# Optimization experiments

Measured on AMD Instinct MI355X. Metric: run time of the kernel, lower is better.

## Reference

```python
import jax, jax.numpy as jnp
import numpy as np

ITERATIONS = 3  # init_kwargs: adjacency power order

def setup_inputs() -> dict:
    key = jax.random.key(0)
    ks = jax.random.split(key, 8)
    n_nodes = 100000
    in_ch, out_ch = 512, 128
    nnz_feat = 1600000
    n_edges = 1600000
    feat_rows = jax.random.randint(ks[0], (nnz_feat,), 0, n_nodes, dtype=jnp.int32)
    feat_cols = jax.random.randint(ks[1], (nnz_feat,), 0, in_ch, dtype=jnp.int32)
    feat_values = jax.random.uniform(ks[2], (nnz_feat,), dtype=jnp.float32)
    adj_rows = jax.random.randint(ks[3], (n_edges,), 0, n_nodes, dtype=jnp.int32)
    adj_cols = jax.random.randint(ks[4], (n_edges,), 0, n_nodes, dtype=jnp.int32)
    # normalized adjacency values (positive, roughly 1/degree scale)
    adj_values = jax.random.uniform(ks[5], (n_edges,), dtype=jnp.float32) / 16.0
    # xavier-uniform-like init
    bound_w = float(np.sqrt(6.0 / (in_ch + out_ch)))
    weight = jax.random.uniform(ks[6], (in_ch, out_ch), minval=-bound_w, maxval=bound_w, dtype=jnp.float32)
    bound_b = float(np.sqrt(6.0 / (1 + out_ch)))
    bias = jax.random.uniform(ks[7], (1, out_ch), minval=-bound_b, maxval=bound_b, dtype=jnp.float32)
    return {"feat_rows": feat_rows, "feat_cols": feat_cols, "feat_values": feat_values,
            "adj_rows": adj_rows, "adj_cols": adj_cols, "adj_values": adj_values,
            "weight": weight, "bias": bias, "n_nodes": n_nodes}

def reference(feat_rows, feat_cols, feat_values, adj_rows, adj_cols, adj_values, weight, bias, n_nodes):
    # SpMM: (sparse features [n_nodes, in_ch]) @ weight [in_ch, out_ch]
    # base[r] = sum over nnz with row r of val * weight[col]
    contrib = feat_values[:, None] * weight[feat_cols]           # [nnz, out_ch]
    base = jax.ops.segment_sum(contrib, feat_rows, num_segments=n_nodes)  # [n_nodes, out_ch]
    # bias + dropout (eval mode: identity) + relu
    base = jax.nn.relu(base + bias)
    # iterative sparse propagation: base = A_norm @ base, (iterations - 1) times
    for _ in range(ITERATIONS - 1):
        msgs = adj_values[:, None] * base[adj_cols]              # [n_edges, out_ch]
        base = jax.ops.segment_sum(msgs, adj_rows, num_segments=n_nodes)
    return base
```

## Files before the change

kernel.cpp:

```cpp
#include <hip/hip_runtime.h>
#include <hip/hip_fp16.h>


#define CH 128
#define BR 128
#define SCAN_BLK 1024
#define BIN_WGS 256
#define BIN_THR 512


__global__ void bucket_hist_kernel(const int* __restrict__ rows, int* __restrict__ bcounts,
                                   int nE, int nbuck, int chunk) {
    extern __shared__ int hcnt[];
    const int tid = threadIdx.x;
    const long long T = blockDim.x;
    long long start = (long long)blockIdx.x * chunk;
    long long end = start + chunk;
    if (end > nE) end = nE;
    for (int b = tid; b < nbuck; b += blockDim.x) hcnt[b] = 0;
    __syncthreads();
    if (start < end) {
        long long i = start + tid;
        for (; i + 3 * T < end; i += 4 * T) {
            int r0 = rows[i], r1 = rows[i + T], r2 = rows[i + 2 * T], r3 = rows[i + 3 * T];
            atomicAdd(&hcnt[r0 >> 7], 1);
            atomicAdd(&hcnt[r1 >> 7], 1);
            atomicAdd(&hcnt[r2 >> 7], 1);
            atomicAdd(&hcnt[r3 >> 7], 1);
        }
        for (; i < end; i += T) atomicAdd(&hcnt[rows[i] >> 7], 1);
    }
    __syncthreads();
    for (int b = tid; b < nbuck; b += blockDim.x) {
        int c = hcnt[b];
        if (c) atomicAdd(&bcounts[b], c);
    }
}

__global__ void bucket_scan_kernel(const int* __restrict__ bcounts, int* __restrict__ bcur,
                                   int* __restrict__ bucket_base, int* __restrict__ row_ptr_n,
                                   int nbuck) {
    __shared__ int lds[SCAN_BLK];
    int tid = threadIdx.x;
    int x = (tid < nbuck) ? bcounts[tid] : 0;
    lds[tid] = x;
    __syncthreads();
    for (int off = 1; off < SCAN_BLK; off <<= 1) {
        int y = (tid >= off) ? lds[tid - off] : 0;
        __syncthreads();
        lds[tid] += y;
        __syncthreads();
    }
    if (tid < nbuck) {
        int excl = lds[tid] - x;
        bcur[tid] = excl;
        bucket_base[tid] = excl;
    }
    if (tid == nbuck - 1) {
        bucket_base[nbuck] = lds[tid];
        *row_ptr_n = lds[tid];
    }
}

__global__ void multisplit_bin_kernel(const int* __restrict__ rows, const int* __restrict__ cols,
                                      const float* __restrict__ vals, int* __restrict__ bcur,
                                      int2* __restrict__ cv_tmp, int nE, int nbuck, int chunk) {
    extern __shared__ int lds[];
    int* hcnt  = lds;
    int* hbase = lds + nbuck;
    const int tid = threadIdx.x;
    const long long T = blockDim.x;
    long long start = (long long)blockIdx.x * chunk;
    long long end = start + chunk;
    if (end > nE) end = nE;
    if (start >= end) return;

    for (int b = tid; b < nbuck; b += blockDim.x) hcnt[b] = 0;
    __syncthreads();
    {
        long long i = start + tid;
        for (; i + 3 * T < end; i += 4 * T) {
            int r0 = rows[i], r1 = rows[i + T], r2 = rows[i + 2 * T], r3 = rows[i + 3 * T];
            atomicAdd(&hcnt[r0 >> 7], 1);
            atomicAdd(&hcnt[r1 >> 7], 1);
            atomicAdd(&hcnt[r2 >> 7], 1);
            atomicAdd(&hcnt[r3 >> 7], 1);
        }
        for (; i < end; i += T) atomicAdd(&hcnt[rows[i] >> 7], 1);
    }
    __syncthreads();
    for (int b = tid; b < nbuck; b += blockDim.x) {
        int c = hcnt[b];
        hbase[b] = c ? atomicAdd(&bcur[b], c) : 0;
        hcnt[b] = 0;
    }
    __syncthreads();
    {
        long long i = start + tid;
        for (; i + 3 * T < end; i += 4 * T) {
            int r0 = rows[i], r1 = rows[i + T], r2 = rows[i + 2 * T], r3 = rows[i + 3 * T];
            int c0 = cols[i], c1 = cols[i + T], c2 = cols[i + 2 * T], c3 = cols[i + 3 * T];
            float v0 = vals[i], v1 = vals[i + T], v2 = vals[i + 2 * T], v3 = vals[i + 3 * T];
            int b0 = r0 >> 7, b1 = r1 >> 7, b2 = r2 >> 7, b3 = r3 >> 7;
            int p0 = hbase[b0] + atomicAdd(&hcnt[b0], 1);
            int p1 = hbase[b1] + atomicAdd(&hcnt[b1], 1);
            int p2 = hbase[b2] + atomicAdd(&hcnt[b2], 1);
            int p3 = hbase[b3] + atomicAdd(&hcnt[b3], 1);
            cv_tmp[p0] = make_int2(c0 | ((r0 & (BR - 1)) << 24), __float_as_int(v0));
            cv_tmp[p1] = make_int2(c1 | ((r1 & (BR - 1)) << 24), __float_as_int(v1));
            cv_tmp[p2] = make_int2(c2 | ((r2 & (BR - 1)) << 24), __float_as_int(v2));
            cv_tmp[p3] = make_int2(c3 | ((r3 & (BR - 1)) << 24), __float_as_int(v3));
        }
        for (; i < end; i += T) {
            int r = rows[i];
            int b = r >> 7;
            int p = hbase[b] + atomicAdd(&hcnt[b], 1);
            cv_tmp[p] = make_int2(cols[i] | ((r & (BR - 1)) << 24), __float_as_int(vals[i]));
        }
    }
}

__global__ void reorder2_kernel(const int* __restrict__ bucket_base,
                                const int2* __restrict__ cv_tmp, int2* __restrict__ cv,
                                int* __restrict__ row_ptr, int n) {
    __shared__ int cnt[BR];
    __shared__ int tmp[BR];
    int b = blockIdx.x;
    int rbase = b * BR;
    int tid = threadIdx.x;
    int s = bucket_base[b], e = bucket_base[b + 1];
    if (tid < BR) cnt[tid] = 0;
    __syncthreads();
    for (int i = s + tid; i < e; i += blockDim.x)
        atomicAdd(&cnt[((unsigned)cv_tmp[i].x) >> 24], 1);
    __syncthreads();
    if (tid < BR) tmp[tid] = cnt[tid];
    __syncthreads();
    for (int off = 1; off < BR; off <<= 1) {
        int y = 0;
        if (tid < BR && tid >= off) y = tmp[tid - off];
        __syncthreads();
        if (tid < BR) tmp[tid] += y;
        __syncthreads();
    }
    if (tid < BR) {
        int excl = s + tmp[tid] - cnt[tid];
        if (rbase + tid < n) row_ptr[rbase + tid] = excl;
        cnt[tid] = excl;
    }
    __syncthreads();
    for (int i = s + tid; i < e; i += blockDim.x) {
        int2 ent = cv_tmp[i];
        int rl = ((unsigned)ent.x) >> 24;
        int p = atomicAdd(&cnt[rl], 1);
        cv[p] = make_int2(ent.x & 0x00FFFFFF, ent.y);
    }
}


__global__ void wconv_kernel(const float* __restrict__ W, __half2* __restrict__ Wh, int n2) {
    int i = blockIdx.x * blockDim.x + threadIdx.x;
    if (i < n2) Wh[i] = __float22half2_rn(reinterpret_cast<const float2*>(W)[i]);
}


__global__ void spmm_g4_kernel(const int* __restrict__ row_ptr,
                               const long long* __restrict__ cv,
                               const __half2* __restrict__ Wh,
                               const float* __restrict__ bias,
                               __half2* __restrict__ outh, int n) {
    __shared__ long long sc[4 * 64];
    int gtid = blockIdx.x * blockDim.x + threadIdx.x;
    int wid = gtid >> 6;
    int lane = gtid & 63;
    if (wid >= n) return;
    int g = lane >> 4;
    int cl = lane & 15;
    long long* mysc = sc + (threadIdx.x >> 6) * 64;
    int s = row_ptr[wid], e = row_ptr[wid + 1];
    float acc0 = 0.f, acc1 = 0.f, acc2 = 0.f, acc3 = 0.f;
    float acc4 = 0.f, acc5 = 0.f, acc6 = 0.f, acc7 = 0.f;
    for (int base = s; base < e; base += 64) {
        int idx = base + lane;
        mysc[lane] = (idx < e) ? cv[idx] : 0;
        int m = e - base; if (m > 64) m = 64;
        for (int k0 = 0; k0 < m; k0 += 4) {
            long long ck = mysc[k0 + g];
            int col = (int)ck;
            float v = __int_as_float((int)(ck >> 32));
            float4 wv = *reinterpret_cast<const float4*>(Wh + (long long)col * 64 + cl * 4);
            float2 f0 = __half22float2(*reinterpret_cast<const __half2*>(&wv.x));
            float2 f1 = __half22float2(*reinterpret_cast<const __half2*>(&wv.y));
            float2 f2 = __half22float2(*reinterpret_cast<const __half2*>(&wv.z));
            float2 f3 = __half22float2(*reinterpret_cast<const __half2*>(&wv.w));
            acc0 += v * f0.x; acc1 += v * f0.y;
            acc2 += v * f1.x; acc3 += v * f1.y;
            acc4 += v * f2.x; acc5 += v * f2.y;
            acc6 += v * f3.x; acc7 += v * f3.y;
        }
    }
    acc0 += __shfl_xor(acc0, 16); acc1 += __shfl_xor(acc1, 16);
    acc2 += __shfl_xor(acc2, 16); acc3 += __shfl_xor(acc3, 16);
    acc4 += __shfl_xor(acc4, 16); acc5 += __shfl_xor(acc5, 16);
    acc6 += __shfl_xor(acc6, 16); acc7 += __shfl_xor(acc7, 16);
    acc0 += __shfl_xor(acc0, 32); acc1 += __shfl_xor(acc1, 32);
    acc2 += __shfl_xor(acc2, 32); acc3 += __shfl_xor(acc3, 32);
    acc4 += __shfl_xor(acc4, 32); acc5 += __shfl_xor(acc5, 32);
    acc6 += __shfl_xor(acc6, 32); acc7 += __shfl_xor(acc7, 32);
    if (g == 0) {
        const float4* bp = reinterpret_cast<const float4*>(bias);
        float4 b0 = bp[cl * 2], b1 = bp[cl * 2 + 1];
        acc0 = fmaxf(acc0 + b0.x, 0.f); acc1 = fmaxf(acc1 + b0.y, 0.f);
        acc2 = fmaxf(acc2 + b0.z, 0.f); acc3 = fmaxf(acc3 + b0.w, 0.f);
        acc4 = fmaxf(acc4 + b1.x, 0.f); acc5 = fmaxf(acc5 + b1.y, 0.f);
        acc6 = fmaxf(acc6 + b1.z, 0.f); acc7 = fmaxf(acc7 + b1.w, 0.f);
        __half2 h0 = __floats2half2_rn(acc0, acc1);
        __half2 h1 = __floats2half2_rn(acc2, acc3);
        __half2 h2 = __floats2half2_rn(acc4, acc5);
        __half2 h3 = __floats2half2_rn(acc6, acc7);
        float4 ov;
        *reinterpret_cast<__half2*>(&ov.x) = h0;
        *reinterpret_cast<__half2*>(&ov.y) = h1;
        *reinterpret_cast<__half2*>(&ov.z) = h2;
        *reinterpret_cast<__half2*>(&ov.w) = h3;
        *reinterpret_cast<float4*>(outh + (long long)wid * 64 + cl * 4) = ov;
    }
}

__global__ void prop_csr_h2h_kernel(const int* __restrict__ row_ptr,
                                    const long long* __restrict__ cv,
                                    const __half2* __restrict__ src, __half2* __restrict__ dst,
                                    int n) {
    __shared__ long long sc[4 * 64];
    int gtid = blockIdx.x * blockDim.x + threadIdx.x;
    int wid = gtid >> 6;
    int lane = gtid & 63;
    if (wid >= n) return;
    long long* mysc = sc + (threadIdx.x >> 6) * 64;
    int s = row_ptr[wid], e = row_ptr[wid + 1];
    float2 acc = {0.0f, 0.0f};
    for (int base = s; base < e; base += 64) {
        int idx = base + lane;
        mysc[lane] = (idx < e) ? cv[idx] : 0;
        int m = e - base; if (m > 64) m = 64;
        for (int k0 = 0; k0 < m; k0 += 8) {
            #pragma unroll
            for (int j = 0; j < 8; j++) {
                long long ck = mysc[k0 + j];
                int col = (int)ck;
                float v = __int_as_float((int)(ck >> 32));
                float2 xf = __half22float2(src[(long long)col * 64 + lane]);
                acc.x += v * xf.x; acc.y += v * xf.y;
            }
        }
    }
    dst[(long long)wid * 64 + lane] = __float22half2_rn(acc);
}

__global__ void prop_csr_h2f_kernel(const int* __restrict__ row_ptr,
                                    const long long* __restrict__ cv,
                                    const __half2* __restrict__ src, float* __restrict__ dst,
                                    int n) {
    __shared__ long long sc[4 * 64];
    int gtid = blockIdx.x * blockDim.x + threadIdx.x;
    int wid = gtid >> 6;
    int lane = gtid & 63;
    if (wid >= n) return;
    long long* mysc = sc + (threadIdx.x >> 6) * 64;
    int s = row_ptr[wid], e = row_ptr[wid + 1];
    float2 acc = {0.0f, 0.0f};
    for (int base = s; base < e; base += 64) {
        int idx = base + lane;
        mysc[lane] = (idx < e) ? cv[idx] : 0;
        int m = e - base; if (m > 64) m = 64;
        for (int k0 = 0; k0 < m; k0 += 8) {
            #pragma unroll
            for (int j = 0; j < 8; j++) {
                long long ck = mysc[k0 + j];
                int col = (int)ck;
                float v = __int_as_float((int)(ck >> 32));
                float2 xf = __half22float2(src[(long long)col * 64 + lane]);
                acc.x += v * xf.x; acc.y += v * xf.y;
            }
        }
    }
    reinterpret_cast<float2*>(dst)[(long long)wid * 64 + lane] = acc;
}


__global__ void bias_relu_kernel(float* __restrict__ buf, const float* __restrict__ bias,
                                 long long total) {
    long long i = ((long long)blockIdx.x * blockDim.x + threadIdx.x) * 4;
    if (i >= total) return;
    float4 v = *reinterpret_cast<float4*>(buf + i);
    int ch = (int)(i & (CH - 1));
    float4 b = *reinterpret_cast<const float4*>(bias + ch);
    v.x = fmaxf(v.x + b.x, 0.0f);
    v.y = fmaxf(v.y + b.y, 0.0f);
    v.z = fmaxf(v.z + b.z, 0.0f);
    v.w = fmaxf(v.w + b.w, 0.0f);
    *reinterpret_cast<float4*>(buf + i) = v;
}

__global__ void spmm_scatter_kernel(const int* __restrict__ rows, const int* __restrict__ cols,
                                    const float* __restrict__ vals, const float* __restrict__ weight,
                                    float* __restrict__ out, int nnz) {
    long long tid = (long long)blockIdx.x * blockDim.x + threadIdx.x;
    if (tid >= (long long)nnz * 32) return;
    int e = (int)(tid >> 5), lane = (int)(tid & 31);
    int r = rows[e], c = cols[e];
    float v = vals[e];
    const float4 w = *reinterpret_cast<const float4*>(weight + (long long)c * CH + lane * 4);
    float* dst = out + (long long)r * CH + lane * 4;
    unsafeAtomicAdd(dst + 0, v * w.x);
    unsafeAtomicAdd(dst + 1, v * w.y);
    unsafeAtomicAdd(dst + 2, v * w.z);
    unsafeAtomicAdd(dst + 3, v * w.w);
}

__global__ void prop_scatter_kernel(const int* __restrict__ rows, const int* __restrict__ cols,
                                    const float* __restrict__ vals, const float* __restrict__ src,
                                    float* __restrict__ dst, int ne) {
    long long tid = (long long)blockIdx.x * blockDim.x + threadIdx.x;
    if (tid >= (long long)ne * 32) return;
    int e = (int)(tid >> 5), lane = (int)(tid & 31);
    int r = rows[e], c = cols[e];
    float v = vals[e];
    const float4 s = *reinterpret_cast<const float4*>(src + (long long)c * CH + lane * 4);
    float* d = dst + (long long)r * CH + lane * 4;
    unsafeAtomicAdd(d + 0, v * s.x);
    unsafeAtomicAdd(d + 1, v * s.y);
    unsafeAtomicAdd(d + 2, v * s.z);
    unsafeAtomicAdd(d + 3, v * s.w);
}


static inline size_t align64(size_t x) { return (x + 63) & ~(size_t)63; }

extern "C" void kernel_launch(void* const* d_in, const int* in_sizes, int n_in,
                              void* d_out, int out_size, void* d_ws, size_t ws_size,
                              hipStream_t stream) {
    const int*   feat_rows = (const int*)d_in[0];
    const int*   feat_cols = (const int*)d_in[1];
    const float* feat_vals = (const float*)d_in[2];
    const int*   adj_rows  = (const int*)d_in[3];
    const int*   adj_cols  = (const int*)d_in[4];
    const float* adj_vals  = (const float*)d_in[5];
    const float* weight    = (const float*)d_in[6];
    const float* bias      = (const float*)d_in[7];

    const int nnz = in_sizes[0];
    const int ne  = in_sizes[3];
    const int n   = out_size / CH;
    const int in_ch = in_sizes[6] / CH;

    float* out = (float*)d_out;
    char*  ws  = (char*)d_ws;

    const size_t NBF = (size_t)n * CH * sizeof(float);
    const size_t NBH = (size_t)n * CH * sizeof(__half);
    const long long total_elems = (long long)n * CH;
    const int BLK = 256;
    const int ew_blocks = (int)((total_elems / 4 + BLK - 1) / BLK);
    const int maxe = nnz > ne ? nnz : ne;
    const int nbuck = (n + BR - 1) / BR;
    const size_t bin_lds = (size_t)nbuck * 2 * sizeof(int);

    size_t off = 0;
    __half2* baseh   = (__half2*)(ws + off); off += align64(NBH);
    __half2* pingh   = (__half2*)(ws + off); off += align64(NBH);
    int*   row_ptr  = (int*)(ws + off);   off += align64(((size_t)n + 1) * 4);
    int*   bcounts  = (int*)(ws + off);   off += align64((size_t)nbuck * 4);
    int*   bcur     = (int*)(ws + off);   off += align64((size_t)nbuck * 4);
    int*   bbase    = (int*)(ws + off);   off += align64(((size_t)nbuck + 1) * 4);
    __half2* Wh     = (__half2*)(ws + off); off += align64((size_t)in_ch * 64 * 4);
    int2*  cv       = (int2*)(ws + off);  off += align64((size_t)maxe * 8);
    int2*  cv_tmp   = (int2*)pingh;
    const bool fast = (ws_size >= off) && (nbuck <= SCAN_BLK) &&
                      (n <= (1 << 24)) && (bin_lds <= 64 * 1024) &&
                      (in_ch <= (1 << 22)) &&
                      ((size_t)maxe * 8 <= NBH);

    if (fast) {
        const int row_blocks = (int)(((long long)n * 64 + BLK - 1) / BLK);
        const int chunk_feat = (nnz + BIN_WGS - 1) / BIN_WGS;
        const int chunk_adj  = (ne + BIN_WGS - 1) / BIN_WGS;
        const int w2 = in_ch * 64;
        const size_t hist_lds = (size_t)nbuck * sizeof(int);

        wconv_kernel<<<(w2 + BLK - 1) / BLK, BLK, 0, stream>>>(weight, Wh, w2);

        hipMemsetAsync(bcounts, 0, (size_t)nbuck * 4, stream);
        bucket_hist_kernel<<<BIN_WGS, BIN_THR, hist_lds, stream>>>(
            feat_rows, bcounts, nnz, nbuck, chunk_feat);
        bucket_scan_kernel<<<1, SCAN_BLK, 0, stream>>>(bcounts, bcur, bbase, row_ptr + n, nbuck);
        multisplit_bin_kernel<<<BIN_WGS, BIN_THR, bin_lds, stream>>>(
            feat_rows, feat_cols, feat_vals, bcur, cv_tmp, nnz, nbuck, chunk_feat);
        reorder2_kernel<<<nbuck, BIN_THR, 0, stream>>>(bbase, cv_tmp, cv, row_ptr, n);
        spmm_g4_kernel<<<row_blocks, BLK, 0, stream>>>(
            row_ptr, (const long long*)cv, Wh, bias, baseh, n);

        hipMemsetAsync(bcounts, 0, (size_t)nbuck * 4, stream);
        bucket_hist_kernel<<<BIN_WGS, BIN_THR, hist_lds, stream>>>(
            adj_rows, bcounts, ne, nbuck, chunk_adj);
        bucket_scan_kernel<<<1, SCAN_BLK, 0, stream>>>(bcounts, bcur, bbase, row_ptr + n, nbuck);
        multisplit_bin_kernel<<<BIN_WGS, BIN_THR, bin_lds, stream>>>(
            adj_rows, adj_cols, adj_vals, bcur, cv_tmp, ne, nbuck, chunk_adj);
        reorder2_kernel<<<nbuck, BIN_THR, 0, stream>>>(bbase, cv_tmp, cv, row_ptr, n);
        prop_csr_h2h_kernel<<<row_blocks, BLK, 0, stream>>>(
            row_ptr, (const long long*)cv, baseh, pingh, n);
        prop_csr_h2f_kernel<<<row_blocks, BLK, 0, stream>>>(
            row_ptr, (const long long*)cv, pingh, out, n);
    } else {
        float* ping = (float*)ws;
        const int spmm_blocks = (int)(((long long)nnz * 32 + BLK - 1) / BLK);
        const int prop_blocks = (int)(((long long)ne * 32 + BLK - 1) / BLK);
        hipMemsetAsync(d_out, 0, NBF, stream);
        spmm_scatter_kernel<<<spmm_blocks, BLK, 0, stream>>>(feat_rows, feat_cols, feat_vals,
                                                             weight, out, nnz);
        bias_relu_kernel<<<ew_blocks, BLK, 0, stream>>>(out, bias, total_elems);
        hipMemsetAsync(ping, 0, NBF, stream);
        prop_scatter_kernel<<<prop_blocks, BLK, 0, stream>>>(adj_rows, adj_cols, adj_vals,
                                                             out, ping, ne);
        hipMemsetAsync(d_out, 0, NBF, stream);
        prop_scatter_kernel<<<prop_blocks, BLK, 0, stream>>>(adj_rows, adj_cols, adj_vals,
                                                             ping, out, ne);
    }
}
```

Before: 259.1 us.

## Store per-workgroup bucket histograms and use 4-edge-per-wave propagation kernels

The binning pipeline now writes per-workgroup bucket histograms and scans them per bucket with wave shuffles. The multisplit kernel can then take deterministic offsets directly instead of rebuilding its histogram and doing global atomics. This removes a full second pass over the row indices, two memsets and the atomic contention. The propagation kernels now split each wave into four groups of 16 lanes that each handle a different edge with 16-byte vector loads, followed by a cross-group shuffle reduction. This gives more independent gathers in flight, at the cost of an extra wgscan launch and the shuffle reduction.

Result: faster. 253.2 us (-2.3%).

```diff
diff --git a/kernel.cpp b/kernel.cpp
--- a/kernel.cpp
+++ b/kernel.cpp
@@ -9,7 +9,7 @@
 #define BIN_THR 512
 
 
-__global__ void bucket_hist_kernel(const int* __restrict__ rows, int* __restrict__ bcounts,
+__global__ void bucket_hist_kernel(const int* __restrict__ rows, int* __restrict__ wg_counts,
                                    int nE, int nbuck, int chunk) {
     extern __shared__ int hcnt[];
     const int tid = threadIdx.x;
@@ -31,13 +31,32 @@
         for (; i < end; i += T) atomicAdd(&hcnt[rows[i] >> 7], 1);
     }
     __syncthreads();
-    for (int b = tid; b < nbuck; b += blockDim.x) {
-        int c = hcnt[b];
-        if (c) atomicAdd(&bcounts[b], c);
-    }
-}
-
-__global__ void bucket_scan_kernel(const int* __restrict__ bcounts, int* __restrict__ bcur,
+    for (int b = tid; b < nbuck; b += blockDim.x)
+        wg_counts[(long long)blockIdx.x * nbuck + b] = hcnt[b];
+}
+
+__global__ void wgscan_kernel(int* __restrict__ wg_counts, int* __restrict__ bcounts,
+                              int nbuck, int nwg) {
+    int b = blockIdx.x * (blockDim.x >> 6) + (threadIdx.x >> 6);
+    int lane = threadIdx.x & 63;
+    if (b >= nbuck) return;
+    int carry = 0;
+    for (int base = 0; base < nwg; base += 64) {
+        int wg = base + lane;
+        int v = (wg < nwg) ? wg_counts[(long long)wg * nbuck + b] : 0;
+        int x = v;
+        #pragma unroll
+        for (int off = 1; off < 64; off <<= 1) {
+            int y = __shfl_up(x, off);
+            if (lane >= off) x += y;
+        }
+        if (wg < nwg) wg_counts[(long long)wg * nbuck + b] = carry + x - v;
+        carry += __shfl(x, 63);
+    }
+    if (lane == 0) bcounts[b] = carry;
+}
+
+__global__ void bucket_scan_kernel(const int* __restrict__ bcounts,
                                    int* __restrict__ bucket_base, int* __restrict__ row_ptr_n,
                                    int nbuck) {
     __shared__ int lds[SCAN_BLK];
@@ -51,11 +70,7 @@
         lds[tid] += y;
         __syncthreads();
     }
-    if (tid < nbuck) {
-        int excl = lds[tid] - x;
-        bcur[tid] = excl;
-        bucket_base[tid] = excl;
-    }
+    if (tid < nbuck) bucket_base[tid] = lds[tid] - x;
     if (tid == nbuck - 1) {
         bucket_base[nbuck] = lds[tid];
         *row_ptr_n = lds[tid];
@@ -63,7 +78,9 @@
 }
 
 __global__ void multisplit_bin_kernel(const int* __restrict__ rows, const int* __restrict__ cols,
-                                      const float* __restrict__ vals, int* __restrict__ bcur,
+                                      const float* __restrict__ vals,
+                                      const int* __restrict__ bbase,
+                                      const int* __restrict__ wg_counts,
                                       int2* __restrict__ cv_tmp, int nE, int nbuck, int chunk) {
     extern __shared__ int lds[];
     int* hcnt  = lds;
@@ -73,50 +90,32 @@
     long long start = (long long)blockIdx.x * chunk;
     long long end = start + chunk;
     if (end > nE) end = nE;
+    for (int b = tid; b < nbuck; b += blockDim.x) {
+        hbase[b] = bbase[b] + wg_counts[(long long)blockIdx.x * nbuck + b];
+        hcnt[b] = 0;
+    }
+    __syncthreads();
     if (start >= end) return;
-
-    for (int b = tid; b < nbuck; b += blockDim.x) hcnt[b] = 0;
-    __syncthreads();
-    {
-        long long i = start + tid;
-        for (; i + 3 * T < end; i += 4 * T) {
-            int r0 = rows[i], r1 = rows[i + T], r2 = rows[i + 2 * T], r3 = rows[i + 3 * T];
-            atomicAdd(&hcnt[r0 >> 7], 1);
-            atomicAdd(&hcnt[r1 >> 7], 1);
-            atomicAdd(&hcnt[r2 >> 7], 1);
-            atomicAdd(&hcnt[r3 >> 7], 1);
-        }
-        for (; i < end; i += T) atomicAdd(&hcnt[rows[i] >> 7], 1);
-    }
-    __syncthreads();
-    for (int b = tid; b < nbuck; b += blockDim.x) {
-        int c = hcnt[b];
-        hbase[b] = c ? atomicAdd(&bcur[b], c) : 0;
-        hcnt[b] = 0;
-    }
-    __syncthreads();
-    {
-        long long i = start + tid;
-        for (; i + 3 * T < end; i += 4 * T) {
-            int r0 = rows[i], r1 = rows[i + T], r2 = rows[i + 2 * T], r3 = rows[i + 3 * T];
-            int c0 = cols[i], c1 = cols[i + T], c2 = cols[i + 2 * T], c3 = cols[i + 3 * T];
-            float v0 = vals[i], v1 = vals[i + T], v2 = vals[i + 2 * T], v3 = vals[i + 3 * T];
-            int b0 = r0 >> 7, b1 = r1 >> 7, b2 = r2 >> 7, b3 = r3 >> 7;
-            int p0 = hbase[b0] + atomicAdd(&hcnt[b0], 1);
-            int p1 = hbase[b1] + atomicAdd(&hcnt[b1], 1);
-            int p2 = hbase[b2] + atomicAdd(&hcnt[b2], 1);
-            int p3 = hbase[b3] + atomicAdd(&hcnt[b3], 1);
-            cv_tmp[p0] = make_int2(c0 | ((r0 & (BR - 1)) << 24), __float_as_int(v0));
-            cv_tmp[p1] = make_int2(c1 | ((r1 & (BR - 1)) << 24), __float_as_int(v1));
-            cv_tmp[p2] = make_int2(c2 | ((r2 & (BR - 1)) << 24), __float_as_int(v2));
-            cv_tmp[p3] = make_int2(c3 | ((r3 & (BR - 1)) << 24), __float_as_int(v3));
-        }
-        for (; i < end; i += T) {
-            int r = rows[i];
-            int b = r >> 7;
-            int p = hbase[b] + atomicAdd(&hcnt[b], 1);
-            cv_tmp[p] = make_int2(cols[i] | ((r & (BR - 1)) << 24), __float_as_int(vals[i]));
-        }
+    long long i = start + tid;
+    for (; i + 3 * T < end; i += 4 * T) {
+        int r0 = rows[i], r1 = rows[i + T], r2 = rows[i + 2 * T], r3 = rows[i + 3 * T];
+        int c0 = cols[i], c1 = cols[i + T], c2 = cols[i + 2 * T], c3 = cols[i + 3 * T];
+        float v0 = vals[i], v1 = vals[i + T], v2 = vals[i + 2 * T], v3 = vals[i + 3 * T];
+        int b0 = r0 >> 7, b1 = r1 >> 7, b2 = r2 >> 7, b3 = r3 >> 7;
+        int p0 = hbase[b0] + atomicAdd(&hcnt[b0], 1);
+        int p1 = hbase[b1] + atomicAdd(&hcnt[b1], 1);
+        int p2 = hbase[b2] + atomicAdd(&hcnt[b2], 1);
+        int p3 = hbase[b3] + atomicAdd(&hcnt[b3], 1);
+        cv_tmp[p0] = make_int2(c0 | ((r0 & (BR - 1)) << 24), __float_as_int(v0));
+        cv_tmp[p1] = make_int2(c1 | ((r1 & (BR - 1)) << 24), __float_as_int(v1));
+        cv_tmp[p2] = make_int2(c2 | ((r2 & (BR - 1)) << 24), __float_as_int(v2));
+        cv_tmp[p3] = make_int2(c3 | ((r3 & (BR - 1)) << 24), __float_as_int(v3));
+    }
+    for (; i < end; i += T) {
+        int r = rows[i];
+        int b = r >> 7;
+        int p = hbase[b] + atomicAdd(&hcnt[b], 1);
+        cv_tmp[p] = make_int2(cols[i] | ((r & (BR - 1)) << 24), __float_as_int(vals[i]));
     }
 }
 
@@ -227,64 +226,111 @@
     }
 }
 
-__global__ void prop_csr_h2h_kernel(const int* __restrict__ row_ptr,
-                                    const long long* __restrict__ cv,
-                                    const __half2* __restrict__ src, __half2* __restrict__ dst,
-                                    int n) {
+__global__ void prop_g4_h2h_kernel(const int* __restrict__ row_ptr,
+                                   const long long* __restrict__ cv,
+                                   const __half2* __restrict__ src, __half2* __restrict__ dst,
+                                   int n) {
     __shared__ long long sc[4 * 64];
     int gtid = blockIdx.x * blockDim.x + threadIdx.x;
     int wid = gtid >> 6;
     int lane = gtid & 63;
     if (wid >= n) return;
+    int g = lane >> 4;
+    int cl = lane & 15;
     long long* mysc = sc + (threadIdx.x >> 6) * 64;
     int s = row_ptr[wid], e = row_ptr[wid + 1];
-    float2 acc = {0.0f, 0.0f};
+    float acc0 = 0.f, acc1 = 0.f, acc2 = 0.f, acc3 = 0.f;
+    float acc4 = 0.f, acc5 = 0.f, acc6 = 0.f, acc7 = 0.f;
     for (int base = s; base < e; base += 64) {
         int idx = base + lane;
         mysc[lane] = (idx < e) ? cv[idx] : 0;
         int m = e - base; if (m > 64) m = 64;
-        for (int k0 = 0; k0 < m; k0 += 8) {
-            #pragma unroll
-            for (int j = 0; j < 8; j++) {
-                long long ck = mysc[k0 + j];
-                int col = (int)ck;
-                float v = __int_as_float((int)(ck >> 32));
-                float2 xf = __half22float2(src[(long long)col * 64 + lane]);
-                acc.x += v * xf.x; acc.y += v * xf.y;
-            }
+        for (int k0 = 0; k0 < m; k0 += 4) {
+            long long ck = mysc[k0 + g];
+            int col = (int)ck;
+            float v = __int_as_float((int)(ck >> 32));
+            float4 sv = *reinterpret_cast<const float4*>(src + (long long)col * 64 + cl * 4);
+            float2 f0 = __half22float2(*reinterpret_cast<const __half2*>(&sv.x));
+            float2 f1 = __half22float2(*reinterpret_cast<const __half2*>(&sv.y));
+            float2 f2 = __half22float2(*reinterpret_cast<const __half2*>(&sv.z));
+            float2 f3 = __half22float2(*reinterpret_cast<const __half2*>(&sv.w));
+            acc0 += v * f0.x; acc1 += v * f0.y;
+            acc2 += v * f1.x; acc3 += v * f1.y;
+            acc4 += v * f2.x; acc5 += v * f2.y;
+            acc6 += v * f3.x; acc7 += v * f3.y;
         }
     }
-    dst[(long long)wid * 64 + lane] = __float22half2_rn(acc);
-}
-
-__global__ void prop_csr_h2f_kernel(const int* __restrict__ row_ptr,
-                                    const long long* __restrict__ cv,
-                                    const __half2* __restrict__ src, float* __restrict__ dst,
-                                    int n) {
+    acc0 += __shfl_xor(acc0, 16); acc1 += __shfl_xor(acc1, 16);
+    acc2 += __shfl_xor(acc2, 16); acc3 += __shfl_xor(acc3, 16);
+    acc4 += __shfl_xor(acc4, 16); acc5 += __shfl_xor(acc5, 16);
+    acc6 += __shfl_xor(acc6, 16); acc7 += __shfl_xor(acc7, 16);
+    acc0 += __shfl_xor(acc0, 32); acc1 += __shfl_xor(acc1, 32);
+    acc2 += __shfl_xor(acc2, 32); acc3 += __shfl_xor(acc3, 32);
+    acc4 += __shfl_xor(acc4, 32); acc5 += __shfl_xor(acc5, 32);
+    acc6 += __shfl_xor(acc6, 32); acc7 += __shfl_xor(acc7, 32);
+    if (g == 0) {
+        __half2 h0 = __floats2half2_rn(acc0, acc1);
+        __half2 h1 = __floats2half2_rn(acc2, acc3);
+        __half2 h2 = __floats2half2_rn(acc4, acc5);
+        __half2 h3 = __floats2half2_rn(acc6, acc7);
+        float4 ov;
+        *reinterpret_cast<__half2*>(&ov.x) = h0;
+        *reinterpret_cast<__half2*>(&ov.y) = h1;
+        *reinterpret_cast<__half2*>(&ov.z) = h2;
+        *reinterpret_cast<__half2*>(&ov.w) = h3;
+        *reinterpret_cast<float4*>(dst + (long long)wid * 64 + cl * 4) = ov;
+    }
+}
+
+__global__ void prop_g4_h2f_kernel(const int* __restrict__ row_ptr,
+                                   const long long* __restrict__ cv,
+                                   const __half2* __restrict__ src, float* __restrict__ dst,
+                                   int n) {
     __shared__ long long sc[4 * 64];
     int gtid = blockIdx.x * blockDim.x + threadIdx.x;
     int wid = gtid >> 6;
     int lane = gtid & 63;
     if (wid >= n) return;
+    int g = lane >> 4;
+    int cl = lane & 15;
     long long* mysc = sc + (threadIdx.x >> 6) * 64;
     int s = row_ptr[wid], e = row_ptr[wid + 1];
-    float2 acc = {0.0f, 0.0f};
+    float acc0 = 0.f, acc1 = 0.f, acc2 = 0.f, acc3 = 0.f;
+    float acc4 = 0.f, acc5 = 0.f, acc6 = 0.f, acc7 = 0.f;
     for (int base = s; base < e; base += 64) {
         int idx = base + lane;
         mysc[lane] = (idx < e) ? cv[idx] : 0;
         int m = e - base; if (m > 64) m = 64;
-        for (int k0 = 0; k0 < m; k0 += 8) {
-            #pragma unroll
-            for (int j = 0; j < 8; j++) {
-                long long ck = mysc[k0 + j];
-                int col = (int)ck;
-                float v = __int_as_float((int)(ck >> 32));
-                float2 xf = __half22float2(src[(long long)col * 64 + lane]);
-                acc.x += v * xf.x; acc.y += v * xf.y;
-            }
+        for (int k0 = 0; k0 < m; k0 += 4) {
+            long long ck = mysc[k0 + g];
+            int col = (int)ck;
+            float v = __int_as_float((int)(ck >> 32));
+            float4 sv = *reinterpret_cast<const float4*>(src + (long long)col * 64 + cl * 4);
+            float2 f0 = __half22float2(*reinterpret_cast<const __half2*>(&sv.x));
+            float2 f1 = __half22float2(*reinterpret_cast<const __half2*>(&sv.y));
+            float2 f2 = __half22float2(*reinterpret_cast<const __half2*>(&sv.z));
+            float2 f3 = __half22float2(*reinterpret_cast<const __half2*>(&sv.w));
+            acc0 += v * f0.x; acc1 += v * f0.y;
+            acc2 += v * f1.x; acc3 += v * f1.y;
+            acc4 += v * f2.x; acc5 += v * f2.y;
+            acc6 += v * f3.x; acc7 += v * f3.y;
         }
     }
-    reinterpret_cast<float2*>(dst)[(long long)wid * 64 + lane] = acc;
+    acc0 += __shfl_xor(acc0, 16); acc1 += __shfl_xor(acc1, 16);
+    acc2 += __shfl_xor(acc2, 16); acc3 += __shfl_xor(acc3, 16);
+    acc4 += __shfl_xor(acc4, 16); acc5 += __shfl_xor(acc5, 16);
+    acc6 += __shfl_xor(acc6, 16); acc7 += __shfl_xor(acc7, 16);
+    acc0 += __shfl_xor(acc0, 32); acc1 += __shfl_xor(acc1, 32);
+    acc2 += __shfl_xor(acc2, 32); acc3 += __shfl_xor(acc3, 32);
+    acc4 += __shfl_xor(acc4, 32); acc5 += __shfl_xor(acc5, 32);
+    acc6 += __shfl_xor(acc6, 32); acc7 += __shfl_xor(acc7, 32);
+    if (g == 0) {
+        float4 o0 = make_float4(acc0, acc1, acc2, acc3);
+        float4 o1 = make_float4(acc4, acc5, acc6, acc7);
+        float4* dp = reinterpret_cast<float4*>(dst + (long long)wid * 128 + cl * 8);
+        dp[0] = o0;
+        dp[1] = o1;
+    }
 }
 
 
@@ -367,15 +413,15 @@
     const size_t bin_lds = (size_t)nbuck * 2 * sizeof(int);
 
     size_t off = 0;
-    __half2* baseh   = (__half2*)(ws + off); off += align64(NBH);
-    __half2* pingh   = (__half2*)(ws + off); off += align64(NBH);
-    int*   row_ptr  = (int*)(ws + off);   off += align64(((size_t)n + 1) * 4);
-    int*   bcounts  = (int*)(ws + off);   off += align64((size_t)nbuck * 4);
-    int*   bcur     = (int*)(ws + off);   off += align64((size_t)nbuck * 4);
-    int*   bbase    = (int*)(ws + off);   off += align64(((size_t)nbuck + 1) * 4);
-    __half2* Wh     = (__half2*)(ws + off); off += align64((size_t)in_ch * 64 * 4);
-    int2*  cv       = (int2*)(ws + off);  off += align64((size_t)maxe * 8);
-    int2*  cv_tmp   = (int2*)pingh;
+    __half2* baseh    = (__half2*)(ws + off); off += align64(NBH);
+    __half2* pingh    = (__half2*)(ws + off); off += align64(NBH);
+    int*   row_ptr   = (int*)(ws + off);   off += align64(((size_t)n + 1) * 4);
+    int*   bcounts   = (int*)(ws + off);   off += align64((size_t)nbuck * 4);
+    int*   bbase     = (int*)(ws + off);   off += align64(((size_t)nbuck + 1) * 4);
+    int*   wg_counts = (int*)(ws + off);   off += align64((size_t)BIN_WGS * nbuck * 4);
+    __half2* Wh      = (__half2*)(ws + off); off += align64((size_t)in_ch * 64 * 4);
+    int2*  cv        = (int2*)(ws + off);  off += align64((size_t)maxe * 8);
+    int2*  cv_tmp    = (int2*)pingh;
     const bool fast = (ws_size >= off) && (nbuck <= SCAN_BLK) &&
                       (n <= (1 << 24)) && (bin_lds <= 64 * 1024) &&
                       (in_ch <= (1 << 22)) &&
@@ -387,29 +433,30 @@
         const int chunk_adj  = (ne + BIN_WGS - 1) / BIN_WGS;
         const int w2 = in_ch * 64;
         const size_t hist_lds = (size_t)nbuck * sizeof(int);
+        const int wgscan_blocks = (nbuck + 3) / 4;
 
         wconv_kernel<<<(w2 + BLK - 1) / BLK, BLK, 0, stream>>>(weight, Wh, w2);
 
-        hipMemsetAsync(bcounts, 0, (size_t)nbuck * 4, stream);
         bucket_hist_kernel<<<BIN_WGS, BIN_THR, hist_lds, stream>>>(
-            feat_rows, bcounts, nnz, nbuck, chunk_feat);
-        bucket_scan_kernel<<<1, SCAN_BLK, 0, stream>>>(bcounts, bcur, bbase, row_ptr + n, nbuck);
+            feat_rows, wg_counts, nnz, nbuck, chunk_feat);
+        wgscan_kernel<<<wgscan_blocks, 256, 0, stream>>>(wg_counts, bcounts, nbuck, BIN_WGS);
+        bucket_scan_kernel<<<1, SCAN_BLK, 0, stream>>>(bcounts, bbase, row_ptr + n, nbuck);
         multisplit_bin_kernel<<<BIN_WGS, BIN_THR, bin_lds, stream>>>(
-            feat_rows, feat_cols, feat_vals, bcur, cv_tmp, nnz, nbuck, chunk_feat);
+            feat_rows, feat_cols, feat_vals, bbase, wg_counts, cv_tmp, nnz, nbuck, chunk_feat);
         reorder2_kernel<<<nbuck, BIN_THR, 0, stream>>>(bbase, cv_tmp, cv, row_ptr, n);
         spmm_g4_kernel<<<row_blocks, BLK, 0, stream>>>(
             row_ptr, (const long long*)cv, Wh, bias, baseh, n);
 
-        hipMemsetAsync(bcounts, 0, (size_t)nbuck * 4, stream);
         bucket_hist_kernel<<<BIN_WGS, BIN_THR, hist_lds, stream>>>(
-            adj_rows, bcounts, ne, nbuck, chunk_adj);
-        bucket_scan_kernel<<<1, SCAN_BLK, 0, stream>>>(bcounts, bcur, bbase, row_ptr + n, nbuck);
+            adj_rows, wg_counts, ne, nbuck, chunk_adj);
+        wgscan_kernel<<<wgscan_blocks, 256, 0, stream>>>(wg_counts, bcounts, nbuck, BIN_WGS);
+        bucket_scan_kernel<<<1, SCAN_BLK, 0, stream>>>(bcounts, bbase, row_ptr + n, nbuck);
         multisplit_bin_kernel<<<BIN_WGS, BIN_THR, bin_lds, stream>>>(
-            adj_rows, adj_cols, adj_vals, bcur, cv_tmp, ne, nbuck, chunk_adj);
+            adj_rows, adj_cols, adj_vals, bbase, wg_counts, cv_tmp, ne, nbuck, chunk_adj);
         reorder2_kernel<<<nbuck, BIN_THR, 0, stream>>>(bbase, cv_tmp, cv, row_ptr, n);
-        prop_csr_h2h_kernel<<<row_blocks, BLK, 0, stream>>>(
+        prop_g4_h2h_kernel<<<row_blocks, BLK, 0, stream>>>(
             row_ptr, (const long long*)cv, baseh, pingh, n);
-        prop_csr_h2f_kernel<<<row_blocks, BLK, 0, stream>>>(
+        prop_g4_h2f_kernel<<<row_blocks, BLK, 0, stream>>>(
             row_ptr, (const long long*)cv, pingh, out, n);
     } else {
         float* ping = (float*)ws;
```
